# Performance work log

Measured on AMD Instinct MI355X. Metric: run time of the kernel, lower is better.

Reference implementation:

```python
import jax, jax.numpy as jnp
import numpy as np

B, S, DIM, H = 4, 4096, 2048, 16
HD = DIM // H  # head_dim = 128


def setup_inputs() -> dict:
    key = jax.random.key(0)
    ks = jax.random.split(key, 6)
    X = jax.random.normal(ks[0], (B, S, DIM), dtype=jnp.float32)
    freqs_cos = jax.random.uniform(ks[1], (S, HD), dtype=jnp.float32)
    freqs_sin = jax.random.uniform(ks[2], (S, HD), dtype=jnp.float32)
    attention_mask = jnp.ones((B, S), dtype=jnp.int32)
    # Linear weights stored as [in, out] (equivalent to torch W.T); no bias.
    scale = 0.02
    Wq = jax.random.normal(ks[3], (DIM, DIM), dtype=jnp.float32) * scale
    Wk = jax.random.normal(ks[4], (DIM, DIM), dtype=jnp.float32) * scale
    Wv = jax.random.normal(ks[5], (DIM, DIM), dtype=jnp.float32) * scale
    return {"X": X, "freqs_cos": freqs_cos, "freqs_sin": freqs_sin,
            "attention_mask": attention_mask, "Wq": Wq, "Wk": Wk, "Wv": Wv}


def _rotate_half_interleaved(x):
    # x: [B, S, H, D]; pairs along last dim: (x0, x1) -> (-x1, x0), interleaved
    xp = x.reshape(*x.shape[:-1], HD // 2, 2)
    xt = jnp.stack([-xp[..., 1], xp[..., 0]], axis=-1)
    return xt.reshape(x.shape)


def reference(X, freqs_cos, freqs_sin, attention_mask, Wq, Wk, Wv):
    bs, seq_len, _ = X.shape
    # QKV projections (no bias), fused view to [B, S, H, HD]
    Xq = (X @ Wq).reshape(bs, seq_len, H, HD)
    Xk = (X @ Wk).reshape(bs, seq_len, H, HD)
    Xv = (X @ Wv).reshape(bs, seq_len, H, HD)
    # RoPE: broadcast freqs to (1, S, 1, HD)
    cos = freqs_cos[None, :, None, :]
    sin = freqs_sin[None, :, None, :]
    Xq_out = Xq * cos + _rotate_half_interleaved(Xq) * sin
    Xk_out = Xk * cos + _rotate_half_interleaved(Xk) * sin
    return (Xq_out, Xk_out, Xv)
```

## Files before the change

### kernel.cpp

```cpp
#include <hip/hip_runtime.h>
#include <hip/hip_bf16.h>
#include <stdint.h>

#define B_    4
#define S_    4096
#define DIM_  2048
#define H_    16
#define HD_   128
#define M_    (B_ * S_)
#define K_    DIM_
#define N_    (3 * DIM_)

typedef __attribute__((ext_vector_type(8))) short bf16x8;
typedef __attribute__((ext_vector_type(4))) float f32x4;

__global__ void cvt_x_kernel(const float* __restrict__ X,
                             __hip_bfloat16* __restrict__ Xb) {
    size_t i = ((size_t)blockIdx.x * 256 + threadIdx.x) * 8;
    float4 a = *reinterpret_cast<const float4*>(X + i);
    float4 b = *reinterpret_cast<const float4*>(X + i + 4);
    union { __hip_bfloat16 h[8]; uint4 u; } o;
    o.h[0] = __float2bfloat16(a.x);
    o.h[1] = __float2bfloat16(a.y);
    o.h[2] = __float2bfloat16(a.z);
    o.h[3] = __float2bfloat16(a.w);
    o.h[4] = __float2bfloat16(b.x);
    o.h[5] = __float2bfloat16(b.y);
    o.h[6] = __float2bfloat16(b.z);
    o.h[7] = __float2bfloat16(b.w);
    *reinterpret_cast<uint4*>(Xb + i) = o.u;
}

__global__ void cvt_w_kernel(const float* __restrict__ Wq,
                             const float* __restrict__ Wk,
                             const float* __restrict__ Wv,
                             __hip_bfloat16* __restrict__ Wt) {
    __shared__ float tile[32][33];
    int w = blockIdx.z;
    const float* W = (w == 0) ? Wq : (w == 1) ? Wk : Wv;
    int n0 = blockIdx.x * 32;
    int k0 = blockIdx.y * 32;
    int tx = threadIdx.x, ty = threadIdx.y;
#pragma unroll
    for (int r = 0; r < 4; ++r) {
        int k = k0 + ty + r * 8;
        tile[ty + r * 8][tx] = W[(size_t)k * DIM_ + n0 + tx];
    }
    __syncthreads();
#pragma unroll
    for (int r = 0; r < 4; ++r) {
        int n = n0 + ty + r * 8;
        Wt[(size_t)(w * DIM_ + n) * K_ + k0 + tx] =
            __float2bfloat16(tile[tx][ty + r * 8]);
    }
}

#define BM 128
#define BN 256
#define BK 32
#define NT (K_ / BK)

#define BAR()      __builtin_amdgcn_s_barrier()
#define WAIT_VM(n) asm volatile("s_waitcnt vmcnt(" #n ")")

__global__ __launch_bounds__(512, 4) void gemm_rope_kernel(
    const __hip_bfloat16* __restrict__ Xb,
    const __hip_bfloat16* __restrict__ Wt,
    const float* __restrict__ fcos,
    const float* __restrict__ fsin,
    float* __restrict__ out)
{
    __shared__ __hip_bfloat16 As[2][BM * BK];
    __shared__ __hip_bfloat16 Bs[2][BN * BK];

    int bid   = blockIdx.x;
    int x     = bid & 7;
    int local = bid >> 3;
    int tn = x * 3 + local % 3;
    int tm = local / 3;
    int m0 = tm * BM, n0 = tn * BN;

    int tid  = threadIdx.x;
    int lane = tid & 63;
    int w    = tid >> 6;
    int wr   = w >> 2;
    int wc   = w & 3;

    int srow = lane >> 2;
    int sgl  = lane & 3;
    int sgs  = (sgl ^ ((lane >> 3) & 3)) * 8;
    int sgd  = sgl * 8;

    int fr = lane & 15;
    int fq = lane >> 4;
    int fk = (fq ^ ((fr >> 1) & 3)) * 8;

#define STAGE_A(t, bb) do {                                                    \
        const __hip_bfloat16* _s = Xb + (size_t)(m0 + w * 16 + srow) * K_      \
                                      + (t) * BK + sgs;                        \
        __hip_bfloat16* _d = &As[bb][(w * 16 + srow) * BK + sgd];              \
        __builtin_amdgcn_global_load_lds(                                      \
            (const __attribute__((address_space(1))) void*)_s,                 \
            (__attribute__((address_space(3))) void*)_d, 16, 0, 0);            \
    } while (0)

#define STAGE_B(t, bb, r) do {                                                 \
        const __hip_bfloat16* _s = Wt + (size_t)(n0 + w * 32 + (r) * 16 + srow) * K_ \
                                      + (t) * BK + sgs;                        \
        __hip_bfloat16* _d = &Bs[bb][(w * 32 + (r) * 16 + srow) * BK + sgd];   \
        __builtin_amdgcn_global_load_lds(                                      \
            (const __attribute__((address_space(1))) void*)_s,                 \
            (__attribute__((address_space(3))) void*)_d, 16, 0, 0);            \
    } while (0)

    f32x4  acc[4][4] = {};
    bf16x8 a[4], b[4];

#define LDA(bb) do {                                                           \
        _Pragma("unroll")                                                      \
        for (int i = 0; i < 4; ++i)                                            \
            a[i] = *reinterpret_cast<const bf16x8*>(                           \
                &As[bb][(wr * 64 + i * 16 + fr) * BK + fk]);                   \
    } while (0)

#define LDB(bb) do {                                                           \
        _Pragma("unroll")                                                      \
        for (int j = 0; j < 4; ++j)                                            \
            b[j] = *reinterpret_cast<const bf16x8*>(                           \
                &Bs[bb][(wc * 64 + j * 16 + fr) * BK + fk]);                   \
    } while (0)

#define MFMA16() do {                                                          \
        __builtin_amdgcn_s_setprio(1);                                         \
        _Pragma("unroll")                                                      \
        for (int i = 0; i < 4; ++i)                                            \
        _Pragma("unroll")                                                      \
        for (int j = 0; j < 4; ++j)                                            \
            acc[i][j] = __builtin_amdgcn_mfma_f32_16x16x32_bf16(               \
                a[i], b[j], acc[i][j], 0, 0, 0);                               \
        __builtin_amdgcn_s_setprio(0);                                         \
    } while (0)

#define TILE(t, P, Q) do {                                                     \
        if ((t) + 1 < NT) {                                                    \
            STAGE_A((t) + 1, Q);                                               \
            STAGE_B((t) + 1, Q, 0); STAGE_B((t) + 1, Q, 1);                    \
        }                                                                      \
        LDA(P); LDB(P);                                                        \
        MFMA16();                                                              \
        WAIT_VM(0);                                                            \
        BAR();                                                                 \
    } while (0)

    STAGE_A(0, 0);
    STAGE_B(0, 0, 0); STAGE_B(0, 0, 1);
    WAIT_VM(0);
    BAR();

    for (int u = 0; u < NT / 2; ++u) {
        TILE(2 * u, 0, 1);
        TILE(2 * u + 1, 1, 0);
    }

#pragma unroll
    for (int i = 0; i < 4; ++i) {
        int mbase = m0 + wr * 64 + i * 16 + fq * 4;
#pragma unroll
        for (int j = 0; j < 4; ++j) {
            int n = n0 + wc * 64 + j * 16 + fr;
            int region = n >> 11;
            int cc = n & (DIM_ - 1);
            int d  = cc & (HD_ - 1);
#pragma unroll
            for (int r = 0; r < 4; ++r) {
                int m = mbase + r;
                int s = m & (S_ - 1);
                float g  = acc[i][j][r];
                float gp = __shfl_xor(g, 1, 64);
                float o;
                if (region < 2) {
                    float cv = fcos[s * HD_ + d];
                    float sv = fsin[s * HD_ + d];
                    o = g * cv + ((cc & 1) ? gp * sv : -gp * sv);
                } else {
                    o = g;
                }
                __builtin_nontemporal_store(
                    o, &out[(size_t)region * M_ * DIM_ + (size_t)m * DIM_ + cc]);
            }
        }
    }
#undef STAGE_A
#undef STAGE_B
#undef LDA
#undef LDB
#undef MFMA16
#undef TILE
}

extern "C" void kernel_launch(void* const* d_in, const int* in_sizes, int n_in,
                              void* d_out, int out_size, void* d_ws, size_t ws_size,
                              hipStream_t stream) {
    const float* X    = (const float*)d_in[0];
    const float* fcos = (const float*)d_in[1];
    const float* fsin = (const float*)d_in[2];
    const float* Wq   = (const float*)d_in[4];
    const float* Wk   = (const float*)d_in[5];
    const float* Wv   = (const float*)d_in[6];
    float* out = (float*)d_out;

    __hip_bfloat16* Xb  = (__hip_bfloat16*)d_ws;
    __hip_bfloat16* Wtp = Xb + (size_t)M_ * K_;

    {
        int threads = 256;
        int blocks = (M_ * K_) / (threads * 8);
        cvt_x_kernel<<<blocks, threads, 0, stream>>>(X, Xb);
    }
    {
        dim3 grid(DIM_ / 32, DIM_ / 32, 3);
        dim3 block(32, 8);
        cvt_w_kernel<<<grid, block, 0, stream>>>(Wq, Wk, Wv, Wtp);
    }
    {
        int blocks = (M_ / BM) * (N_ / BN);
        gemm_rope_kernel<<<blocks, 512, 0, stream>>>(Xb, Wtp, fcos, fsin, out);
    }
}
```

Before: 523.8 us.

## Load B operand directly from global into registers, bypassing LDS

New measurement: 899.0 us. 71.6% more time.

```diff
diff --git a/kernel.cpp b/kernel.cpp
--- a/kernel.cpp
+++ b/kernel.cpp
@@ -62,6 +62,7 @@
 
 #define BAR()      __builtin_amdgcn_s_barrier()
 #define WAIT_VM(n) asm volatile("s_waitcnt vmcnt(" #n ")")
+#define SCHEDB()   __builtin_amdgcn_sched_barrier(0)
 
 __global__ __launch_bounds__(512, 4) void gemm_rope_kernel(
     const __hip_bfloat16* __restrict__ Xb,
@@ -71,7 +72,6 @@
     float* __restrict__ out)
 {
     __shared__ __hip_bfloat16 As[2][BM * BK];
-    __shared__ __hip_bfloat16 Bs[2][BN * BK];
 
     int bid   = blockIdx.x;
     int x     = bid & 7;
@@ -94,6 +94,8 @@
     int fr = lane & 15;
     int fq = lane >> 4;
     int fk = (fq ^ ((fr >> 1) & 3)) * 8;
+
+    const __hip_bfloat16* pB = Wt + (size_t)(n0 + wc * 64 + fr) * K_ + fq * 8;
 
 #define STAGE_A(t, bb) do {                                                    \
         const __hip_bfloat16* _s = Xb + (size_t)(m0 + w * 16 + srow) * K_      \
@@ -104,15 +106,6 @@
             (__attribute__((address_space(3))) void*)_d, 16, 0, 0);            \
     } while (0)
 
-#define STAGE_B(t, bb, r) do {                                                 \
-        const __hip_bfloat16* _s = Wt + (size_t)(n0 + w * 32 + (r) * 16 + srow) * K_ \
-                                      + (t) * BK + sgs;                        \
-        __hip_bfloat16* _d = &Bs[bb][(w * 32 + (r) * 16 + srow) * BK + sgd];   \
-        __builtin_amdgcn_global_load_lds(                                      \
-            (const __attribute__((address_space(1))) void*)_s,                 \
-            (__attribute__((address_space(3))) void*)_d, 16, 0, 0);            \
-    } while (0)
-
     f32x4  acc[4][4] = {};
     bf16x8 a[4], b[4];
 
@@ -123,38 +116,35 @@
                 &As[bb][(wr * 64 + i * 16 + fr) * BK + fk]);                   \
     } while (0)
 
-#define LDB(bb) do {                                                           \
-        _Pragma("unroll")                                                      \
-        for (int j = 0; j < 4; ++j)                                            \
-            b[j] = *reinterpret_cast<const bf16x8*>(                           \
-                &Bs[bb][(wc * 64 + j * 16 + fr) * BK + fk]);                   \
-    } while (0)
-
-#define MFMA16() do {                                                          \
+#define LDB_J(j, t)                                                            \
+        b[j] = *reinterpret_cast<const bf16x8*>(                               \
+            pB + (size_t)(j) * 16 * K_ + (t) * BK)
+
+#define TILE(t, P, Q) do {                                                     \
+        if ((t) + 1 < NT) STAGE_A((t) + 1, Q);                                 \
+        SCHEDB();                       \
+        LDA(P);                                                                \
         __builtin_amdgcn_s_setprio(1);                                         \
         _Pragma("unroll")                                                      \
-        for (int i = 0; i < 4; ++i)                                            \
-        _Pragma("unroll")                                                      \
-        for (int j = 0; j < 4; ++j)                                            \
-            acc[i][j] = __builtin_amdgcn_mfma_f32_16x16x32_bf16(               \
-                a[i], b[j], acc[i][j], 0, 0, 0);                               \
+        for (int j = 0; j < 4; ++j) {                                          \
+            _Pragma("unroll")                                                  \
+            for (int i = 0; i < 4; ++i)                                        \
+                acc[i][j] = __builtin_amdgcn_mfma_f32_16x16x32_bf16(           \
+                    a[i], b[j], acc[i][j], 0, 0, 0);                           \
+            if ((t) + 1 < NT) LDB_J(j, (t) + 1);                               \
+        }                                                                      \
         __builtin_amdgcn_s_setprio(0);                                         \
-    } while (0)
-
-#define TILE(t, P, Q) do {                                                     \
-        if ((t) + 1 < NT) {                                                    \
-            STAGE_A((t) + 1, Q);                                               \
-            STAGE_B((t) + 1, Q, 0); STAGE_B((t) + 1, Q, 1);                    \
-        }                                                                      \
-        LDA(P); LDB(P);                                                        \
-        MFMA16();                                                              \
-        WAIT_VM(0);                                                            \
+        SCHEDB();                             \
+        if ((t) + 1 < NT) { WAIT_VM(4); }                                      \
         BAR();                                                                 \
     } while (0)
 
     STAGE_A(0, 0);
-    STAGE_B(0, 0, 0); STAGE_B(0, 0, 1);
-    WAIT_VM(0);
+    SCHEDB();
+#pragma unroll
+    for (int j = 0; j < 4; ++j) LDB_J(j, 0);
+    SCHEDB();
+    WAIT_VM(4);
     BAR();
 
     for (int u = 0; u < NT / 2; ++u) {
@@ -191,10 +181,8 @@
         }
     }
 #undef STAGE_A
-#undef STAGE_B
 #undef LDA
-#undef LDB
-#undef MFMA16
+#undef LDB_J
 #undef TILE
 }
 
```

## Halve GEMM M tile to 64 and split B fragment loads across two phases

Applied to the files above, without the earlier changes.

After: 750.1 us. 43.2% more time.

```diff
diff --git a/kernel.cpp b/kernel.cpp
--- a/kernel.cpp
+++ b/kernel.cpp
@@ -55,7 +55,7 @@
     }
 }
 
-#define BM 128
+#define BM 64
 #define BN 256
 #define BK 32
 #define NT (K_ / BK)
@@ -63,7 +63,7 @@
 #define BAR()      __builtin_amdgcn_s_barrier()
 #define WAIT_VM(n) asm volatile("s_waitcnt vmcnt(" #n ")")
 
-__global__ __launch_bounds__(512, 4) void gemm_rope_kernel(
+__global__ __launch_bounds__(512, 8) void gemm_rope_kernel(
     const __hip_bfloat16* __restrict__ Xb,
     const __hip_bfloat16* __restrict__ Wt,
     const float* __restrict__ fcos,
@@ -96,12 +96,14 @@
     int fk = (fq ^ ((fr >> 1) & 3)) * 8;
 
 #define STAGE_A(t, bb) do {                                                    \
-        const __hip_bfloat16* _s = Xb + (size_t)(m0 + w * 16 + srow) * K_      \
-                                      + (t) * BK + sgs;                        \
-        __hip_bfloat16* _d = &As[bb][(w * 16 + srow) * BK + sgd];              \
-        __builtin_amdgcn_global_load_lds(                                      \
-            (const __attribute__((address_space(1))) void*)_s,                 \
-            (__attribute__((address_space(3))) void*)_d, 16, 0, 0);            \
+        if (w < 4) {                                                           \
+            const __hip_bfloat16* _s = Xb + (size_t)(m0 + w * 16 + srow) * K_  \
+                                          + (t) * BK + sgs;                    \
+            __hip_bfloat16* _d = &As[bb][(w * 16 + srow) * BK + sgd];          \
+            __builtin_amdgcn_global_load_lds(                                  \
+                (const __attribute__((address_space(1))) void*)_s,             \
+                (__attribute__((address_space(3))) void*)_d, 16, 0, 0);        \
+        }                                                                      \
     } while (0)
 
 #define STAGE_B(t, bb, r) do {                                                 \
@@ -113,32 +115,30 @@
             (__attribute__((address_space(3))) void*)_d, 16, 0, 0);            \
     } while (0)
 
-    f32x4  acc[4][4] = {};
-    bf16x8 a[4], b[4];
+    f32x4  acc[2][4] = {};
+    bf16x8 a2[2], b2[2];
 
 #define LDA(bb) do {                                                           \
         _Pragma("unroll")                                                      \
-        for (int i = 0; i < 4; ++i)                                            \
-            a[i] = *reinterpret_cast<const bf16x8*>(                           \
-                &As[bb][(wr * 64 + i * 16 + fr) * BK + fk]);                   \
-    } while (0)
-
-#define LDB(bb) do {                                                           \
-        _Pragma("unroll")                                                      \
-        for (int j = 0; j < 4; ++j)                                            \
-            b[j] = *reinterpret_cast<const bf16x8*>(                           \
-                &Bs[bb][(wc * 64 + j * 16 + fr) * BK + fk]);                   \
-    } while (0)
-
-#define MFMA16() do {                                                          \
-        __builtin_amdgcn_s_setprio(1);                                         \
-        _Pragma("unroll")                                                      \
-        for (int i = 0; i < 4; ++i)                                            \
-        _Pragma("unroll")                                                      \
-        for (int j = 0; j < 4; ++j)                                            \
-            acc[i][j] = __builtin_amdgcn_mfma_f32_16x16x32_bf16(               \
-                a[i], b[j], acc[i][j], 0, 0, 0);                               \
-        __builtin_amdgcn_s_setprio(0);                                         \
+        for (int i = 0; i < 2; ++i)                                            \
+            a2[i] = *reinterpret_cast<const bf16x8*>(                          \
+                &As[bb][(wr * 32 + i * 16 + fr) * BK + fk]);                   \
+    } while (0)
+
+#define LDB2(bb, j0) do {                                                      \
+        _Pragma("unroll")                                                      \
+        for (int j = 0; j < 2; ++j)                                            \
+            b2[j] = *reinterpret_cast<const bf16x8*>(                          \
+                &Bs[bb][(wc * 64 + ((j0) + j) * 16 + fr) * BK + fk]);          \
+    } while (0)
+
+#define MFMA2(j0) do {                                                         \
+        _Pragma("unroll")                                                      \
+        for (int j = 0; j < 2; ++j)                                            \
+        _Pragma("unroll")                                                      \
+        for (int i = 0; i < 2; ++i)                                            \
+            acc[i][(j0) + j] = __builtin_amdgcn_mfma_f32_16x16x32_bf16(        \
+                a2[i], b2[j], acc[i][(j0) + j], 0, 0, 0);                      \
     } while (0)
 
 #define TILE(t, P, Q) do {                                                     \
@@ -146,8 +146,15 @@
             STAGE_A((t) + 1, Q);                                               \
             STAGE_B((t) + 1, Q, 0); STAGE_B((t) + 1, Q, 1);                    \
         }                                                                      \
-        LDA(P); LDB(P);                                                        \
-        MFMA16();                                                              \
+        LDA(P);                                                                \
+        LDB2(P, 0);                                                            \
+        __builtin_amdgcn_s_setprio(1);                                         \
+        MFMA2(0);                                                              \
+        __builtin_amdgcn_s_setprio(0);                                         \
+        LDB2(P, 2);                                                            \
+        __builtin_amdgcn_s_setprio(1);                                         \
+        MFMA2(2);                                                              \
+        __builtin_amdgcn_s_setprio(0);                                         \
         WAIT_VM(0);                                                            \
         BAR();                                                                 \
     } while (0)
@@ -163,8 +170,8 @@
     }
 
 #pragma unroll
-    for (int i = 0; i < 4; ++i) {
-        int mbase = m0 + wr * 64 + i * 16 + fq * 4;
+    for (int i = 0; i < 2; ++i) {
+        int mbase = m0 + wr * 32 + i * 16 + fq * 4;
 #pragma unroll
         for (int j = 0; j < 4; ++j) {
             int n = n0 + wc * 64 + j * 16 + fr;
@@ -193,8 +200,8 @@
 #undef STAGE_A
 #undef STAGE_B
 #undef LDA
-#undef LDB
-#undef MFMA16
+#undef LDB2
+#undef MFMA2
 #undef TILE
 }
 
```

## Use 256x128 block tile with 4 waves each computing 128x64 outputs

Applied to the files above, without the earlier changes.

Measured after the change: 1.135 ms. +116.7%, slower.

```diff
diff --git a/kernel.cpp b/kernel.cpp
--- a/kernel.cpp
+++ b/kernel.cpp
@@ -55,15 +55,15 @@
     }
 }
 
-#define BM 128
-#define BN 256
+#define BM 256
+#define BN 128
 #define BK 32
 #define NT (K_ / BK)
 
 #define BAR()      __builtin_amdgcn_s_barrier()
 #define WAIT_VM(n) asm volatile("s_waitcnt vmcnt(" #n ")")
 
-__global__ __launch_bounds__(512, 4) void gemm_rope_kernel(
+__global__ __launch_bounds__(256, 3) void gemm_rope_kernel(
     const __hip_bfloat16* __restrict__ Xb,
     const __hip_bfloat16* __restrict__ Wt,
     const float* __restrict__ fcos,
@@ -76,15 +76,15 @@
     int bid   = blockIdx.x;
     int x     = bid & 7;
     int local = bid >> 3;
-    int tn = x * 3 + local % 3;
-    int tm = local / 3;
+    int tn = x * 6 + local % 6;
+    int tm = local / 6;
     int m0 = tm * BM, n0 = tn * BN;
 
     int tid  = threadIdx.x;
     int lane = tid & 63;
     int w    = tid >> 6;
-    int wr   = w >> 2;
-    int wc   = w & 3;
+    int wr   = w >> 1;
+    int wc   = w & 1;
 
     int srow = lane >> 2;
     int sgl  = lane & 3;
@@ -95,10 +95,10 @@
     int fq = lane >> 4;
     int fk = (fq ^ ((fr >> 1) & 3)) * 8;
 
-#define STAGE_A(t, bb) do {                                                    \
-        const __hip_bfloat16* _s = Xb + (size_t)(m0 + w * 16 + srow) * K_      \
+#define STAGE_A(t, bb, r) do {                                                 \
+        const __hip_bfloat16* _s = Xb + (size_t)(m0 + w * 64 + (r) * 16 + srow) * K_ \
                                       + (t) * BK + sgs;                        \
-        __hip_bfloat16* _d = &As[bb][(w * 16 + srow) * BK + sgd];              \
+        __hip_bfloat16* _d = &As[bb][(w * 64 + (r) * 16 + srow) * BK + sgd];   \
         __builtin_amdgcn_global_load_lds(                                      \
             (const __attribute__((address_space(1))) void*)_s,                 \
             (__attribute__((address_space(3))) void*)_d, 16, 0, 0);            \
@@ -113,15 +113,8 @@
             (__attribute__((address_space(3))) void*)_d, 16, 0, 0);            \
     } while (0)
 
-    f32x4  acc[4][4] = {};
-    bf16x8 a[4], b[4];
-
-#define LDA(bb) do {                                                           \
-        _Pragma("unroll")                                                      \
-        for (int i = 0; i < 4; ++i)                                            \
-            a[i] = *reinterpret_cast<const bf16x8*>(                           \
-                &As[bb][(wr * 64 + i * 16 + fr) * BK + fk]);                   \
-    } while (0)
+    f32x4  acc[8][4] = {};
+    bf16x8 a4[4], b[4];
 
 #define LDB(bb) do {                                                           \
         _Pragma("unroll")                                                      \
@@ -130,29 +123,40 @@
                 &Bs[bb][(wc * 64 + j * 16 + fr) * BK + fk]);                   \
     } while (0)
 
-#define MFMA16() do {                                                          \
+#define LDA4(bb, ih) do {                                                      \
+        _Pragma("unroll")                                                      \
+        for (int ii = 0; ii < 4; ++ii)                                         \
+            a4[ii] = *reinterpret_cast<const bf16x8*>(                         \
+                &As[bb][(wr * 128 + ((ih) * 4 + ii) * 16 + fr) * BK + fk]);    \
+    } while (0)
+
+#define MFMA_H(ih) do {                                                        \
         __builtin_amdgcn_s_setprio(1);                                         \
         _Pragma("unroll")                                                      \
-        for (int i = 0; i < 4; ++i)                                            \
+        for (int ii = 0; ii < 4; ++ii)                                         \
         _Pragma("unroll")                                                      \
         for (int j = 0; j < 4; ++j)                                            \
-            acc[i][j] = __builtin_amdgcn_mfma_f32_16x16x32_bf16(               \
-                a[i], b[j], acc[i][j], 0, 0, 0);                               \
+            acc[(ih) * 4 + ii][j] = __builtin_amdgcn_mfma_f32_16x16x32_bf16(   \
+                a4[ii], b[j], acc[(ih) * 4 + ii][j], 0, 0, 0);                 \
         __builtin_amdgcn_s_setprio(0);                                         \
     } while (0)
 
 #define TILE(t, P, Q) do {                                                     \
         if ((t) + 1 < NT) {                                                    \
-            STAGE_A((t) + 1, Q);                                               \
+            STAGE_A((t) + 1, Q, 0); STAGE_A((t) + 1, Q, 1);                    \
+            STAGE_A((t) + 1, Q, 2); STAGE_A((t) + 1, Q, 3);                    \
             STAGE_B((t) + 1, Q, 0); STAGE_B((t) + 1, Q, 1);                    \
         }                                                                      \
-        LDA(P); LDB(P);                                                        \
-        MFMA16();                                                              \
+        LDB(P);                                                                \
+        LDA4(P, 0);                                                            \
+        MFMA_H(0);                                                             \
+        LDA4(P, 1);                                                            \
+        MFMA_H(1);                                                             \
         WAIT_VM(0);                                                            \
         BAR();                                                                 \
     } while (0)
 
-    STAGE_A(0, 0);
+    STAGE_A(0, 0, 0); STAGE_A(0, 0, 1); STAGE_A(0, 0, 2); STAGE_A(0, 0, 3);
     STAGE_B(0, 0, 0); STAGE_B(0, 0, 1);
     WAIT_VM(0);
     BAR();
@@ -163,8 +167,8 @@
     }
 
 #pragma unroll
-    for (int i = 0; i < 4; ++i) {
-        int mbase = m0 + wr * 64 + i * 16 + fq * 4;
+    for (int i = 0; i < 8; ++i) {
+        int mbase = m0 + wr * 128 + i * 16 + fq * 4;
 #pragma unroll
         for (int j = 0; j < 4; ++j) {
             int n = n0 + wc * 64 + j * 16 + fr;
@@ -192,9 +196,9 @@
     }
 #undef STAGE_A
 #undef STAGE_B
-#undef LDA
 #undef LDB
-#undef MFMA16
+#undef LDA4
+#undef MFMA_H
 #undef TILE
 }
 
@@ -224,6 +228,6 @@
     }
     {
         int blocks = (M_ / BM) * (N_ / BN);
-        gemm_rope_kernel<<<blocks, 512, 0, stream>>>(Xb, Wtp, fcos, fsin, out);
-    }
-}
+        gemm_rope_kernel<<<blocks, 256, 0, stream>>>(Xb, Wtp, fcos, fsin, out);
+    }
+}
```
